# Kernel optimization log

Measured on AMD Instinct MI355X. Metric: run time of the kernel, lower is better.

The kernel has to match this reference:

```python
import jax, jax.numpy as jnp
import numpy as np

B, S, D, H = 4, 2048, 1024, 16
HS = D // H  # head size = 64


def setup_inputs() -> dict:
    key = jax.random.key(0)
    k1, k2, k3 = jax.random.split(key, 3)
    return {
        "input_data": jax.random.normal(k1, (B, S, D), dtype=jnp.float32),
        "w_qkv": jax.random.normal(k2, (D, 3 * D), dtype=jnp.float32) * (1.0 / np.sqrt(D)),
        "b_qkv": jnp.zeros((3 * D,), dtype=jnp.float32),
        "w_proj": jax.random.normal(k3, (D, D), dtype=jnp.float32) * (1.0 / np.sqrt(D)),
        "b_proj": jnp.zeros((D,), dtype=jnp.float32),
    }


def reference(input_data, w_qkv, b_qkv, w_proj, b_proj):
    b, s, d = input_data.shape
    qkv = input_data @ w_qkv + b_qkv  # [b, s, 3d]
    q, k, v = jnp.split(qkv, 3, axis=-1)
    # [b, h, s, hs]
    q = q.reshape(b, s, H, HS).transpose(0, 2, 1, 3)
    k = k.reshape(b, s, H, HS).transpose(0, 2, 1, 3)
    v = v.reshape(b, s, H, HS).transpose(0, 2, 1, 3)
    # NB: original module scales by 1/sqrt(num_heads), not 1/sqrt(head_size)
    scores = jnp.einsum('bhqd,bhkd->bhqk', q, k) / jnp.sqrt(jnp.float32(H))
    causal = jnp.tril(jnp.ones((s, s), dtype=bool))
    scores = jnp.where(causal[None, None], scores, -jnp.inf)
    weights = jax.nn.softmax(scores, axis=-1)  # dropout p=0.0 -> identity
    out = jnp.einsum('bhqk,bhkd->bhqd', weights, v)
    out = out.transpose(0, 2, 1, 3).reshape(b, s, d)
    return out @ w_proj + b_proj
```

## Files before the change

### kernel.cpp

```cpp
#include <hip/hip_runtime.h>


typedef unsigned short u16;
typedef short bf16x8 __attribute__((ext_vector_type(8)));
typedef unsigned short u16x8 __attribute__((ext_vector_type(8)));
typedef float f32x4 __attribute__((ext_vector_type(4)));
typedef float f32x16 __attribute__((ext_vector_type(16)));

#define S_LEN 2048
#define DMODEL 1024
#define NHEAD 16
#define MROWS 8192

#define SCALE_LOG2E 0.36067376022224085f

#define WAITVM_(N) asm volatile("s_waitcnt vmcnt(" #N ")" ::: "memory")
#define WAITVM(N) WAITVM_(N)

__device__ __forceinline__ u16 f2bf(float f) {
  union { float f; unsigned u; } c; c.f = f;
  unsigned u = c.u;
  u += 0x7fffu + ((u >> 16) & 1u);
  return (u16)(u >> 16);
}

__device__ __forceinline__ float exp2_fast(float x) {
  float r; asm("v_exp_f32 %0, %1" : "=v"(r) : "v"(x)); return r;
}

__device__ __forceinline__ unsigned cvtpk_bf16(float a, float b) {
  unsigned r;
  asm("v_cvt_pk_bf16_f32 %0, %1, %2" : "=v"(r) : "v"(a), "v"(b));
  return r;
}

__device__ __forceinline__ void plswap(unsigned& a, unsigned& b) {
  asm("v_permlane32_swap_b32 %0, %1" : "+v"(a), "+v"(b));
}

__device__ __forceinline__ f32x4 mfma16(bf16x8 a, bf16x8 b, f32x4 c) {
  return __builtin_amdgcn_mfma_f32_16x16x32_bf16(a, b, c, 0, 0, 0);
}

__device__ __forceinline__ f32x16 mfma32(bf16x8 a, bf16x8 b, f32x16 c) {
  return __builtin_amdgcn_mfma_f32_32x32x16_bf16(a, b, c, 0, 0, 0);
}

__device__ __forceinline__ void gload_lds16(const void* g, void* l) {
  __builtin_amdgcn_global_load_lds((__attribute__((address_space(1))) void*)g,
                                   (__attribute__((address_space(3))) void*)l,
                                   16, 0, 0);
}

__global__ void k_f32_to_bf16(const float* __restrict__ in, u16* __restrict__ out, int n) {
  int i = (blockIdx.x * 256 + threadIdx.x) * 4;
  if (i < n) {
    float4 v = *reinterpret_cast<const float4*>(in + i);
    ushort4 o;
    o.x = f2bf(v.x); o.y = f2bf(v.y); o.z = f2bf(v.z); o.w = f2bf(v.w);
    *reinterpret_cast<ushort4*>(out + i) = o;
  }
}

__global__ void k_transpose_to_bf16(const float* __restrict__ in, u16* __restrict__ out,
                                    int K, int N) {
  __shared__ float t[32][33];
  int n0 = blockIdx.x * 32, k0 = blockIdx.y * 32;
  int tx = threadIdx.x & 31, ty = threadIdx.x >> 5;
#pragma unroll
  for (int i = 0; i < 32; i += 8)
    t[ty + i][tx] = in[(size_t)(k0 + ty + i) * N + n0 + tx];
  __syncthreads();
#pragma unroll
  for (int i = 0; i < 32; i += 8)
    out[(size_t)(n0 + ty + i) * K + k0 + tx] = f2bf(t[tx][ty + i]);
}

template <int MODE>
__global__ __launch_bounds__(512, 1) void k_gemm8(const u16* __restrict__ A,
                                                  const u16* __restrict__ Bt,
                                                  const float* __restrict__ bias,
                                                  u16* __restrict__ outb,
                                                  float* __restrict__ outf,
                                                  u16* __restrict__ vtout,
                                                  int N, int K) {
  __shared__ u16 As[3][2][256 * 32];
  __shared__ u16 Bs[3][2][128 * 32];

  const int tid = threadIdx.x;
  const int lane = tid & 63, wave = tid >> 6;
  const int wr = wave >> 1, wc = wave & 1;
  const int lr = lane & 15, lk = lane >> 4;
  const int m0 = blockIdx.x * 256, n0 = blockIdx.y * 128;
  const size_t Kb = (size_t)K * 2;

  const int csw = ((tid & 3) ^ ((tid >> 3) & 3)) * 16;
  const char* Asrc0 = (const char*)A + (size_t)(m0 + (tid >> 2)) * Kb + csw;
  const char* Asrc1 = Asrc0 + 128 * Kb;
  const char* Bsrc0 = (const char*)Bt + (size_t)(n0 + (tid >> 2)) * Kb + csw;

#define STAGE_KH(BUFX, KH, T)                                                  \
  {                                                                            \
    const size_t ko_ = (size_t)(T) * 128 + (KH) * 64;                          \
    gload_lds16(Asrc0 + ko_, &As[BUFX][KH][(size_t)tid * 8]);                  \
    gload_lds16(Asrc1 + ko_, &As[BUFX][KH][((size_t)tid + 512) * 8]);          \
    gload_lds16(Bsrc0 + ko_, &Bs[BUFX][KH][(size_t)tid * 8]);                  \
  }

  f32x4 zero4 = {0.f, 0.f, 0.f, 0.f};
  f32x4 acc[4][4];
#pragma unroll
  for (int m = 0; m < 4; ++m)
#pragma unroll
    for (int n = 0; n < 4; ++n) acc[m][n] = zero4;

  const int slotsw = (lr >> 1) & 3;

#define PHASE(BUFX, KH, VM, DOSTAGE, SBUF, ST)                                 \
  {                                                                            \
    WAITVM(VM);                                                                \
    __builtin_amdgcn_s_barrier();                                              \
    __builtin_amdgcn_sched_barrier(0);                                         \
    bf16x8 af[4], bfr[4];                                                      \
    _Pragma("unroll") for (int m = 0; m < 4; ++m)                              \
        af[m] = *reinterpret_cast<const bf16x8*>(                              \
            &As[BUFX][KH][(wr * 64 + m * 16 + lr) * 32 + ((lk ^ slotsw) * 8)]);\
    _Pragma("unroll") for (int n = 0; n < 4; ++n)                              \
        bfr[n] = *reinterpret_cast<const bf16x8*>(                             \
            &Bs[BUFX][KH][(wc * 64 + n * 16 + lr) * 32 + ((lk ^ slotsw) * 8)]);\
    if (DOSTAGE) STAGE_KH(SBUF, KH, ST);                                       \
    __builtin_amdgcn_sched_barrier(0);                                         \
    __builtin_amdgcn_s_setprio(1);                                             \
    _Pragma("unroll") for (int m = 0; m < 4; ++m)                              \
        _Pragma("unroll") for (int n = 0; n < 4; ++n)                          \
            acc[m][n] = mfma16(af[m], bfr[n], acc[m][n]);                      \
    __builtin_amdgcn_s_setprio(0);                                             \
  }

  const int nkt = K >> 6;
  STAGE_KH(0, 0, 0);
  STAGE_KH(0, 1, 0);
  STAGE_KH(1, 0, 1);
  STAGE_KH(1, 1, 1);

  for (int t = 0; t < nkt - 2; ++t) {
    const int bf3 = t % 3;
    const int bn3 = (t + 2) % 3;
    PHASE(bf3, 0, 6, 1, bn3, t + 2);
    PHASE(bf3, 1, 9, 1, bn3, t + 2);
  }
  {
    const int bf3 = (nkt - 2) % 3;
    PHASE(bf3, 0, 6, 0, 0, 0);
    PHASE(bf3, 1, 6, 0, 0, 0);
  }
  {
    const int bf3 = (nkt - 1) % 3;
    PHASE(bf3, 0, 0, 0, 0, 0);
    PHASE(bf3, 1, 0, 0, 0, 0);
  }
#undef PHASE
#undef STAGE_KH

#pragma unroll
  for (int n = 0; n < 4; ++n) {
    int col = n0 + wc * 64 + n * 16 + lr;
    float bv = bias[col];
#pragma unroll
    for (int m = 0; m < 4; ++m) {
      int rowb = m0 + wr * 64 + m * 16 + lk * 4;
      if (MODE == 1) {
#pragma unroll
        for (int r = 0; r < 4; ++r)
          outf[(size_t)(rowb + r) * N + col] = acc[m][n][r] + bv;
      } else {
        if (col < 2048) {
          const float qs = (col < 1024) ? SCALE_LOG2E : 1.0f;
#pragma unroll
          for (int r = 0; r < 4; ++r)
            outb[(size_t)(rowb + r) * 2048 + col] = f2bf((acc[m][n][r] + bv) * qs);
        } else {
          int hh = (col >> 6) & 15, dd = col & 63;
          int bb = rowb >> 11, ss = rowb & 2047;
          ushort4 o;
          o.x = f2bf(acc[m][n][0] + bv);
          o.y = f2bf(acc[m][n][1] + bv);
          o.z = f2bf(acc[m][n][2] + bv);
          o.w = f2bf(acc[m][n][3] + bv);
          *reinterpret_cast<ushort4*>(
              vtout + ((size_t)(bb * 16 + hh) * 64 + dd) * 2048 + ss) = o;
        }
      }
    }
  }
}

__global__ __launch_bounds__(256, 2) void k_attn14(const u16* __restrict__ qk,
                                                   const u16* __restrict__ vt,
                                                   u16* __restrict__ ao) {
  __shared__ u16 Ks[2][4096];
  __shared__ u16 Vs[2][4096];

  const int tid = threadIdx.x;
  const int lane = tid & 63, wave = tid >> 6;
  const int l31 = lane & 31, hi = lane >> 5;
  const int gid = blockIdx.x;
  const int bh = gid & 63;
  const int tq = gid >> 6;
  const int j = (tq < 4) ? tq : 11 - tq;
  const int b = bh >> 4, h = bh & 15;

  const int qbase = j * 256 + wave * 64;
  const int ktd = 4 * j + wave;
  const int KTMAX = 4 * j + 3;

  bf16x8 qf[2][4];
#pragma unroll
  for (int g = 0; g < 2; ++g) {
    const u16* qp = qk + ((size_t)b * S_LEN + qbase + g * 32 + l31) * 2048 + h * 64 + hi * 8;
#pragma unroll
    for (int ks = 0; ks < 4; ++ks)
      qf[g][ks] = *reinterpret_cast<const bf16x8*>(qp + ks * 16);
  }

  const int swzcol = 16 * ((lane & 7) ^ (lane >> 3));
  const char* kg = (const char*)qk + ((size_t)b * S_LEN) * 4096 + 2048 + h * 128 +
                   (size_t)(wave * 16 + (lane >> 3)) * 4096 + swzcol;
  const char* vg = (const char*)vt +
                   ((size_t)bh * 64 + wave * 16 + (lane >> 3)) * 4096 + swzcol;

#define STAGE(BUF, KT)                                                        \
  {                                                                           \
    const char* kg_ = kg + (size_t)(KT) * 64 * 4096;                          \
    const char* vg_ = vg + (size_t)(KT) * 128;                                \
    gload_lds16(kg_, &Ks[BUF][wave * 1024]);                                  \
    gload_lds16(kg_ + (size_t)8 * 4096, &Ks[BUF][wave * 1024 + 512]);         \
    gload_lds16(vg_, &Vs[BUF][wave * 1024]);                                  \
    gload_lds16(vg_ + (size_t)8 * 4096, &Vs[BUF][wave * 1024 + 512]);         \
  }

  f32x16 oT[2][2];
#pragma unroll
  for (int g = 0; g < 2; ++g)
#pragma unroll
    for (int kb = 0; kb < 2; ++kb)
#pragma unroll
      for (int e = 0; e < 16; ++e) oT[g][kb][e] = 0.f;
  float l_i[2] = {0.f, 0.f};

  const int rsw = (l31 & 7) << 4;

  STAGE(0, 0);
  __syncthreads();
  int buf = 0;

  for (int kt = 0; kt <= KTMAX; ++kt) {
    if (kt < KTMAX) STAGE(buf ^ 1, kt + 1);

    if (kt <= ktd) {
      const char* Kb = (const char*)&Ks[buf][0];
      const char* Vb = (const char*)&Vs[buf][0];
      const bool masked = (kt == ktd);

      bf16x8 kf[2][4];
#pragma unroll
      for (int kb = 0; kb < 2; ++kb)
#pragma unroll
        for (int ks = 0; ks < 4; ++ks)
          kf[kb][ks] = *reinterpret_cast<const bf16x8*>(
              Kb + (kb * 32 + l31) * 128 + ((ks * 32 + hi * 16) ^ rsw));

      bf16x8 vf[2][4];
#pragma unroll
      for (int kbd = 0; kbd < 2; ++kbd)
#pragma unroll
        for (int tt = 0; tt < 4; ++tt)
          vf[kbd][tt] = *reinterpret_cast<const bf16x8*>(
              Vb + (kbd * 32 + l31) * 128 + ((tt * 32 + hi * 16) ^ rsw));

#pragma unroll
      for (int g = 0; g < 2; ++g) {
        f32x16 sc[2];
        __builtin_amdgcn_s_setprio(1);
#pragma unroll
        for (int kb = 0; kb < 2; ++kb) {
          sc[kb] = mfma32(kf[kb][0], qf[g][0], f32x16{});
#pragma unroll
          for (int ks = 1; ks < 4; ++ks)
            sc[kb] = mfma32(kf[kb][ks], qf[g][ks], sc[kb]);
        }
        __builtin_amdgcn_s_setprio(0);

        if (masked) {
          const int qrel = g * 32 + l31;
#pragma unroll
          for (int kb = 0; kb < 2; ++kb)
#pragma unroll
            for (int e = 0; e < 16; ++e) {
              int key_ = kb * 32 + (e & 3) + ((e >> 2) << 3) + hi * 4;
              if (key_ > qrel) sc[kb][e] = -INFINITY;
            }
        }

        float rsa = 0.f, rsb = 0.f, rsc = 0.f, rsd = 0.f;
        unsigned pk_[8][2];
#pragma unroll
        for (int kb = 0; kb < 2; ++kb)
#pragma unroll
          for (int s = 0; s < 4; ++s) {
            float p0 = exp2_fast(sc[kb][s * 4 + 0]);
            float p1 = exp2_fast(sc[kb][s * 4 + 1]);
            float p2 = exp2_fast(sc[kb][s * 4 + 2]);
            float p3 = exp2_fast(sc[kb][s * 4 + 3]);
            rsa += p0; rsb += p1; rsc += p2; rsd += p3;
            pk_[kb * 4 + s][0] = cvtpk_bf16(p0, p1);
            pk_[kb * 4 + s][1] = cvtpk_bf16(p2, p3);
          }
        l_i[g] += (rsa + rsb) + (rsc + rsd);

        bf16x8 pfr[4];
#pragma unroll
        for (int tt = 0; tt < 4; ++tt) {
          unsigned a0 = pk_[2 * tt][0], b0 = pk_[2 * tt + 1][0];
          unsigned a1 = pk_[2 * tt][1], b1 = pk_[2 * tt + 1][1];
          plswap(a0, b0);
          plswap(a1, b1);
          unsigned fr[4] = {a0, a1, b0, b1};
          pfr[tt] = *reinterpret_cast<const bf16x8*>(&fr[0]);
        }

        __builtin_amdgcn_s_setprio(1);
#pragma unroll
        for (int tt = 0; tt < 4; ++tt) {
          oT[g][0] = mfma32(vf[0][tt], pfr[tt], oT[g][0]);
          oT[g][1] = mfma32(vf[1][tt], pfr[tt], oT[g][1]);
        }
        __builtin_amdgcn_s_setprio(0);
      }
    }

    __syncthreads();
    buf ^= 1;
  }
#undef STAGE

#pragma unroll
  for (int g = 0; g < 2; ++g) {
    float lt = l_i[g] + __shfl_xor(l_i[g], 32, 64);
    float inv = 1.f / lt;
    u16* orow = ao + ((size_t)b * S_LEN + qbase + g * 32 + l31) * DMODEL + h * 64 + hi * 4;
#pragma unroll
    for (int kbd = 0; kbd < 2; ++kbd)
#pragma unroll
      for (int s = 0; s < 4; ++s) {
        unsigned w0 = cvtpk_bf16(oT[g][kbd][s * 4 + 0] * inv, oT[g][kbd][s * 4 + 1] * inv);
        unsigned w1 = cvtpk_bf16(oT[g][kbd][s * 4 + 2] * inv, oT[g][kbd][s * 4 + 3] * inv);
        *reinterpret_cast<unsigned*>(orow + kbd * 32 + s * 8) = w0;
        *reinterpret_cast<unsigned*>(orow + kbd * 32 + s * 8 + 2) = w1;
      }
  }
}

extern "C" void kernel_launch(void* const* d_in, const int* in_sizes, int n_in,
                              void* d_out, int out_size, void* d_ws, size_t ws_size,
                              hipStream_t stream) {
  const float* x = (const float*)d_in[0];
  const float* wqkv = (const float*)d_in[1];
  const float* bqkv = (const float*)d_in[2];
  const float* wproj = (const float*)d_in[3];
  const float* bproj = (const float*)d_in[4];
  float* out = (float*)d_out;

  char* ws = (char*)d_ws;
  u16* Xb     = (u16*)(ws);
  u16* Wqkvt  = (u16*)(ws + (size_t)16777216);
  u16* Wprojt = (u16*)(ws + (size_t)23068672);
  u16* QKb    = (u16*)(ws + (size_t)25165824);
  u16* Vt     = (u16*)(ws + (size_t)58720256);
  u16* AOb    = (u16*)(ws + (size_t)75497472);

  k_f32_to_bf16<<<MROWS * DMODEL / 4 / 256, 256, 0, stream>>>(x, Xb, MROWS * DMODEL);
  k_transpose_to_bf16<<<dim3(3072 / 32, 1024 / 32), 256, 0, stream>>>(wqkv, Wqkvt, 1024, 3072);
  k_transpose_to_bf16<<<dim3(1024 / 32, 1024 / 32), 256, 0, stream>>>(wproj, Wprojt, 1024, 1024);

  k_gemm8<2><<<dim3(MROWS / 256, 3072 / 128), 512, 0, stream>>>(
      Xb, Wqkvt, bqkv, QKb, nullptr, Vt, 3072, 1024);

  k_attn14<<<dim3(512), 256, 0, stream>>>(QKb, Vt, AOb);

  k_gemm8<1><<<dim3(MROWS / 256, DMODEL / 128), 512, 0, stream>>>(
      AOb, Wprojt, bproj, nullptr, out, nullptr, DMODEL, 1024);
}
```

Baseline: 172.3 us.

## Template GEMM on block-M and use 128-row tiles for output projection

The GEMM is templated on the M tile size and the K pipeline changes from 64-wide tiles split into two halves to single 32-wide stages with triple buffering. The output projection now runs with 128x128 tiles and 256 threads, doubling its grid to 512 blocks for better CU coverage on a 1024-wide output, and drops the one-block-per-CU launch bound. The trade is more barriers per K step and less operand reuse per block, and the 128-row variant adds an extra B load per stage.

Result: no change. 171.6 us (-0.4%).

```diff
diff --git a/kernel.cpp b/kernel.cpp
--- a/kernel.cpp
+++ b/kernel.cpp
@@ -76,35 +76,39 @@
     out[(size_t)(n0 + ty + i) * K + k0 + tx] = f2bf(t[tx][ty + i]);
 }
 
-template <int MODE>
-__global__ __launch_bounds__(512, 1) void k_gemm8(const u16* __restrict__ A,
+template <int MODE, int BM>
+__global__ __launch_bounds__(BM * 2) void k_gemm9(const u16* __restrict__ A,
                                                   const u16* __restrict__ Bt,
                                                   const float* __restrict__ bias,
                                                   u16* __restrict__ outb,
                                                   float* __restrict__ outf,
                                                   u16* __restrict__ vtout,
                                                   int N, int K) {
-  __shared__ u16 As[3][2][256 * 32];
-  __shared__ u16 Bs[3][2][128 * 32];
+  constexpr int LOADS = (BM == 256) ? 3 : 4;
+  __shared__ u16 As[3][BM * 32];
+  __shared__ u16 Bs[3][128 * 32];
 
   const int tid = threadIdx.x;
   const int lane = tid & 63, wave = tid >> 6;
   const int wr = wave >> 1, wc = wave & 1;
   const int lr = lane & 15, lk = lane >> 4;
-  const int m0 = blockIdx.x * 256, n0 = blockIdx.y * 128;
+  const int m0 = blockIdx.x * BM, n0 = blockIdx.y * 128;
   const size_t Kb = (size_t)K * 2;
 
   const int csw = ((tid & 3) ^ ((tid >> 3) & 3)) * 16;
   const char* Asrc0 = (const char*)A + (size_t)(m0 + (tid >> 2)) * Kb + csw;
-  const char* Asrc1 = Asrc0 + 128 * Kb;
+  const char* Asrc1 = Asrc0 + (size_t)(BM / 2) * Kb;
   const char* Bsrc0 = (const char*)Bt + (size_t)(n0 + (tid >> 2)) * Kb + csw;
-
-#define STAGE_KH(BUFX, KH, T)                                                  \
+  const char* Bsrc1 = Bsrc0 + (size_t)64 * Kb;
+
+#define STAGE_T(BUFX, T)                                                       \
   {                                                                            \
-    const size_t ko_ = (size_t)(T) * 128 + (KH) * 64;                          \
-    gload_lds16(Asrc0 + ko_, &As[BUFX][KH][(size_t)tid * 8]);                  \
-    gload_lds16(Asrc1 + ko_, &As[BUFX][KH][((size_t)tid + 512) * 8]);          \
-    gload_lds16(Bsrc0 + ko_, &Bs[BUFX][KH][(size_t)tid * 8]);                  \
+    const size_t ko_ = (size_t)(T) * 64;                                       \
+    gload_lds16(Asrc0 + ko_, &As[BUFX][(size_t)tid * 8]);                      \
+    gload_lds16(Asrc1 + ko_, &As[BUFX][(size_t)tid * 8 + (size_t)BM * 16]);    \
+    gload_lds16(Bsrc0 + ko_, &Bs[BUFX][(size_t)tid * 8]);                      \
+    if (BM == 128)                                                             \
+      gload_lds16(Bsrc1 + ko_, &Bs[BUFX][(size_t)tid * 8 + 2048]);             \
   }
 
   f32x4 zero4 = {0.f, 0.f, 0.f, 0.f};
@@ -116,19 +120,21 @@
 
   const int slotsw = (lr >> 1) & 3;
 
-#define PHASE(BUFX, KH, VM, DOSTAGE, SBUF, ST)                                 \
+#define PHASE_T(BUFX, DOSTAGE, SBUF, ST, VMZERO)                               \
   {                                                                            \
-    WAITVM(VM);                                                                \
+    if (VMZERO) { WAITVM(0); }                                                 \
+    else if (LOADS == 3) { WAITVM(3); }                                        \
+    else { WAITVM(4); }                                                        \
     __builtin_amdgcn_s_barrier();                                              \
     __builtin_amdgcn_sched_barrier(0);                                         \
     bf16x8 af[4], bfr[4];                                                      \
     _Pragma("unroll") for (int m = 0; m < 4; ++m)                              \
         af[m] = *reinterpret_cast<const bf16x8*>(                              \
-            &As[BUFX][KH][(wr * 64 + m * 16 + lr) * 32 + ((lk ^ slotsw) * 8)]);\
+            &As[BUFX][(wr * 64 + m * 16 + lr) * 32 + ((lk ^ slotsw) * 8)]);    \
     _Pragma("unroll") for (int n = 0; n < 4; ++n)                              \
         bfr[n] = *reinterpret_cast<const bf16x8*>(                             \
-            &Bs[BUFX][KH][(wc * 64 + n * 16 + lr) * 32 + ((lk ^ slotsw) * 8)]);\
-    if (DOSTAGE) STAGE_KH(SBUF, KH, ST);                                       \
+            &Bs[BUFX][(wc * 64 + n * 16 + lr) * 32 + ((lk ^ slotsw) * 8)]);    \
+    if (DOSTAGE) STAGE_T(SBUF, ST);                                            \
     __builtin_amdgcn_sched_barrier(0);                                         \
     __builtin_amdgcn_s_setprio(1);                                             \
     _Pragma("unroll") for (int m = 0; m < 4; ++m)                              \
@@ -137,30 +143,17 @@
     __builtin_amdgcn_s_setprio(0);                                             \
   }
 
-  const int nkt = K >> 6;
-  STAGE_KH(0, 0, 0);
-  STAGE_KH(0, 1, 0);
-  STAGE_KH(1, 0, 1);
-  STAGE_KH(1, 1, 1);
+  const int nkt = K >> 5;
+  STAGE_T(0, 0);
+  STAGE_T(1, 1);
 
   for (int t = 0; t < nkt - 2; ++t) {
-    const int bf3 = t % 3;
-    const int bn3 = (t + 2) % 3;
-    PHASE(bf3, 0, 6, 1, bn3, t + 2);
-    PHASE(bf3, 1, 9, 1, bn3, t + 2);
-  }
-  {
-    const int bf3 = (nkt - 2) % 3;
-    PHASE(bf3, 0, 6, 0, 0, 0);
-    PHASE(bf3, 1, 6, 0, 0, 0);
-  }
-  {
-    const int bf3 = (nkt - 1) % 3;
-    PHASE(bf3, 0, 0, 0, 0, 0);
-    PHASE(bf3, 1, 0, 0, 0, 0);
-  }
-#undef PHASE
-#undef STAGE_KH
+    PHASE_T(t % 3, 1, (t + 2) % 3, t + 2, 0);
+  }
+  PHASE_T((nkt - 2) % 3, 0, 0, 0, 0);
+  PHASE_T((nkt - 1) % 3, 0, 0, 0, 1);
+#undef PHASE_T
+#undef STAGE_T
 
 #pragma unroll
   for (int n = 0; n < 4; ++n) {
@@ -383,11 +376,11 @@
   k_transpose_to_bf16<<<dim3(3072 / 32, 1024 / 32), 256, 0, stream>>>(wqkv, Wqkvt, 1024, 3072);
   k_transpose_to_bf16<<<dim3(1024 / 32, 1024 / 32), 256, 0, stream>>>(wproj, Wprojt, 1024, 1024);
 
-  k_gemm8<2><<<dim3(MROWS / 256, 3072 / 128), 512, 0, stream>>>(
+  k_gemm9<2, 256><<<dim3(MROWS / 256, 3072 / 128), 512, 0, stream>>>(
       Xb, Wqkvt, bqkv, QKb, nullptr, Vt, 3072, 1024);
 
   k_attn14<<<dim3(512), 256, 0, stream>>>(QKb, Vt, AOb);
 
-  k_gemm8<1><<<dim3(MROWS / 256, DMODEL / 128), 512, 0, stream>>>(
+  k_gemm9<1, 128><<<dim3(MROWS / 128, DMODEL / 128), 256, 0, stream>>>(
       AOb, Wprojt, bproj, nullptr, out, nullptr, DMODEL, 1024);
 }
```
